# Optimization experiments

Hardware: AMD Instinct MI355X
Metric: run time of the kernel (lower is better)

Reference implementation:

```python
import math
import jax, jax.numpy as jnp
import numpy as np

H = 12
D = 64  # head dim

def _heads(x):
    # [b, n, h*d] -> [b, h, n, d]
    b, n, _ = x.shape
    return x.reshape(b, n, H, D).transpose(0, 2, 1, 3)

def setup_inputs() -> dict:
    key = jax.random.key(0)
    ks = jax.random.split(key, 9)
    hs = 768
    s = 1.0 / math.sqrt(hs)
    return {
        "query_states": jax.random.normal(ks[0], (8, 1024, hs), jnp.float32),
        "key_states": jax.random.normal(ks[1], (8, 1024, hs), jnp.float32),
        "Wd": jax.random.normal(ks[2], (hs, hs), jnp.float32) * s,
        "Wq": jax.random.normal(ks[3], (hs, hs), jnp.float32) * s,
        "bq": jax.random.normal(ks[4], (hs,), jnp.float32) * 0.01,
        "Wk": jax.random.normal(ks[5], (hs, hs), jnp.float32) * s,
        "bk": jax.random.normal(ks[6], (hs,), jnp.float32) * 0.01,
        "Wv": jax.random.normal(ks[7], (hs, hs), jnp.float32) * s,
        "bv": jax.random.normal(ks[8], (hs,), jnp.float32) * 0.01,
    }

def reference(query_states, key_states, Wd, Wq, bq, Wk, bk, Wv, bv):
    # projections (torch Linear: x @ W.T + b)
    qd = _heads(query_states @ Wd.T)          # [b,h,n,d]
    kd = _heads(key_states @ Wd.T)
    q = _heads(query_states @ Wq.T + bq)
    k = _heads(key_states @ Wk.T + bk)
    v = _heads(key_states @ Wv.T + bv)
    # -0.5 * cdist(qd, kd)^2 = -0.5*(|qd|^2 + |kd|^2) + qd@kd^T
    qd_sq = jnp.sum(qd * qd, axis=-1)          # [b,h,n]
    kd_sq = jnp.sum(kd * kd, axis=-1)          # [b,h,m]
    quad = (qd @ jnp.swapaxes(kd, -1, -2)
            - 0.5 * qd_sq[..., :, None]
            - 0.5 * kd_sq[..., None, :])       # [b,h,n,m]
    lin = q @ jnp.swapaxes(k, -1, -2)          # [b,h,n,m]
    scores = (quad + lin) / math.sqrt(D)
    probs = jax.nn.softmax(scores, axis=-1)
    ctx = probs @ v                            # [b,h,n,d]
    b, _, n, _ = ctx.shape
    return ctx.transpose(0, 2, 1, 3).reshape(b, n, H * D)
```

## Files before the change

### kernel.cpp

```cpp
#include <hip/hip_runtime.h>
#include <stdint.h>

typedef __attribute__((ext_vector_type(8))) short short8;
typedef __attribute__((ext_vector_type(4))) short short4v;
typedef __attribute__((ext_vector_type(4))) float f32x4;
typedef __attribute__((ext_vector_type(16))) float f32x16;
typedef __attribute__((ext_vector_type(4))) int int4v;

static __device__ __forceinline__ unsigned short f2b(float f) {
  unsigned int u = __builtin_bit_cast(unsigned int, f);
  u += 0x7fffu + ((u >> 16) & 1u);
  return (unsigned short)(u >> 16);
}
static __device__ __forceinline__ float b2f(unsigned short b) {
  unsigned int u = ((unsigned int)b) << 16;
  return __builtin_bit_cast(float, u);
}

#define GLD16(gp, lp)                                                          \
  __builtin_amdgcn_global_load_lds(                                            \
      (const __attribute__((address_space(1))) void*)(gp),                     \
      (__attribute__((address_space(3))) void*)(lp), 16, 0, 0)

#define MFMA16 __builtin_amdgcn_mfma_f32_16x16x32_bf16
#define MFMA32 __builtin_amdgcn_mfma_f32_32x32x16_bf16

#define CVTPK(dst, lo, hi)                                                     \
  asm("v_cvt_pk_bf16_f32 %0, %1, %2" : "=v"(dst) : "v"(lo), "v"(hi))
#define PLSWAP(x, y)                                                           \
  asm volatile("v_permlane32_swap_b32 %0, %1" : "+v"(x), "+v"(y))

#define QSC 0.18033688011112113f
#define C2 0.09016844005556057f

__global__ void cvtx_kernel(const float* __restrict__ q,
                            const float* __restrict__ k,
                            unsigned short* __restrict__ Xq,
                            unsigned short* __restrict__ Xk) {
  const int bx = blockIdx.x;
  const bool lo = bx < 6144;
  const float* src = lo ? q : k;
  unsigned short* dst = lo ? Xq : Xk;
  const int i = (lo ? bx : bx - 6144) * 256 + threadIdx.x;
  float4 v = reinterpret_cast<const float4*>(src)[i];
  short4v o;
  o.x = (short)f2b(v.x);
  o.y = (short)f2b(v.y);
  o.z = (short)f2b(v.z);
  o.w = (short)f2b(v.w);
  reinterpret_cast<short4v*>(dst)[i] = o;
}

__global__ void cvtw_kernel(const float* __restrict__ Wd,
                            const float* __restrict__ Wq,
                            const float* __restrict__ Wk,
                            const float* __restrict__ Wv,
                            unsigned short* __restrict__ Wcq,
                            unsigned short* __restrict__ Wck) {
  const int bx = blockIdx.x;
  const int seg = bx / 576;
  const int i = (bx - seg * 576) * 256 + threadIdx.x;
  const float* src;
  unsigned short* dst;
  switch (seg) {
    case 0: src = Wd; dst = Wcq; break;
    case 1: src = Wq; dst = Wcq + 589824; break;
    case 2: src = Wd; dst = Wck; break;
    case 3: src = Wk; dst = Wck + 589824; break;
    default: src = Wv; dst = Wck + 1179648; break;
  }
  float4 v = reinterpret_cast<const float4*>(src)[i];
  short4v o;
  o.x = (short)f2b(v.x);
  o.y = (short)f2b(v.y);
  o.z = (short)f2b(v.z);
  o.w = (short)f2b(v.w);
  reinterpret_cast<short4v*>(dst)[i] = o;
}

__global__ __launch_bounds__(512, 2) void proj_kernel(
    const unsigned short* __restrict__ Xq, const unsigned short* __restrict__ Xk,
    const unsigned short* __restrict__ Wcq, const unsigned short* __restrict__ Wck,
    const float* __restrict__ bq, const float* __restrict__ bk,
    const float* __restrict__ bv, unsigned short* __restrict__ Qc,
    unsigned short* __restrict__ Kc, unsigned short* __restrict__ Vt) {
  __shared__ __align__(16) short lds[3][2][256 * 32];
  const int by = blockIdx.y;
  const bool mode0 = (by < 6);
  const unsigned short* X = mode0 ? Xq : Xk;
  const unsigned short* W = mode0 ? Wcq : Wck;
  const int col0 = (mode0 ? by : by - 6) * 256;
  const int row0 = blockIdx.x * 256;
  const int tid = threadIdx.x;
  const int lane = tid & 63;
  const int wid = tid >> 6;
  const int wm = wid >> 2;
  const int wn = wid & 3;
  const int l15 = lane & 15, l4 = lane >> 4;
  const int RSWZ = (l4 ^ ((l15 >> 1) & 3)) << 4;

  f32x4 acc[8][4];
#pragma unroll
  for (int i = 0; i < 8; ++i)
#pragma unroll
    for (int j = 0; j < 4; ++j) acc[i][j] = (f32x4){0.f, 0.f, 0.f, 0.f};

  auto stage = [&](int bufi, int k0) {
#pragma unroll
    for (int iss = 0; iss < 2; ++iss) {
      const int c = iss * 512 + tid;
      const int r = c >> 2;
      const int sl = (c & 3) ^ ((c >> 3) & 3);
      const unsigned short* gp = X + (size_t)(row0 + r) * 768 + k0 + sl * 8;
      GLD16(gp, (char*)&lds[bufi][0][0] + (size_t)c * 16);
    }
#pragma unroll
    for (int iss = 0; iss < 2; ++iss) {
      const int c = iss * 512 + tid;
      const int r = c >> 2;
      const int sl = (c & 3) ^ ((c >> 3) & 3);
      const unsigned short* gp = W + (size_t)(col0 + r) * 768 + k0 + sl * 8;
      GLD16(gp, (char*)&lds[bufi][1][0] + (size_t)c * 16);
    }
  };

  stage(0, 0);
  stage(1, 32);

#pragma unroll 3
  for (int kt = 0; kt < 24; ++kt) {
    if (kt < 23) {
      asm volatile("s_waitcnt vmcnt(4) lgkmcnt(0)" ::: "memory");
    } else {
      asm volatile("s_waitcnt vmcnt(0) lgkmcnt(0)" ::: "memory");
    }
    __builtin_amdgcn_s_barrier();
    asm volatile("" ::: "memory");
    if (kt < 22) stage((kt + 2) % 3, (kt + 2) * 32);

    const char* Ab = (const char*)&lds[kt % 3][0][0];
    const char* Bb = (const char*)&lds[kt % 3][1][0];
    short8 a[8], b[4];
#pragma unroll
    for (int mt = 0; mt < 8; ++mt) {
      const int r = wm * 128 + mt * 16 + l15;
      a[mt] = *reinterpret_cast<const short8*>(Ab + r * 64 + RSWZ);
    }
#pragma unroll
    for (int nt = 0; nt < 4; ++nt) {
      const int r = wn * 64 + nt * 16 + l15;
      b[nt] = *reinterpret_cast<const short8*>(Bb + r * 64 + RSWZ);
    }
#pragma unroll
    for (int mt = 0; mt < 8; ++mt)
#pragma unroll
      for (int nt = 0; nt < 4; ++nt)
        acc[mt][nt] = MFMA16(a[mt], b[nt], acc[mt][nt], 0, 0, 0);
  }

  const int mat = mode0 ? (col0 >= 768 ? 1 : 0) : ((by - 6) / 3);
  const int cbase = col0 - mat * 768 + wn * 64;
  const float* barr = mode0 ? bq : (mat == 2 ? bv : bk);
  if (!mode0 && mat == 2) {
#pragma unroll
    for (int nt = 0; nt < 4; ++nt) {
      const int cc = cbase + nt * 16 + l15;
      const int hh = cc >> 6, dd = cc & 63;
      const float bias = barr[cc];
#pragma unroll
      for (int mt = 0; mt < 8; ++mt) {
        const int row = row0 + wm * 128 + mt * 16 + l4 * 4;
        const int bb = row >> 10, nn = row & 1023;
        short4v pv;
#pragma unroll
        for (int i = 0; i < 4; ++i)
          pv[i] = (short)f2b(acc[mt][nt][i] + bias);
        *reinterpret_cast<short4v*>(
            Vt + ((size_t)(bb * 12 + hh) * 64 + dd) * 1024 + nn) = pv;
      }
    }
  } else {
    const float scale = mode0 ? QSC : 1.0f;
    unsigned short* outC = mode0 ? Qc : Kc;
#pragma unroll
    for (int nt = 0; nt < 4; ++nt) {
      const int cc = cbase + nt * 16 + l15;
      const int hh = cc >> 6, dd = cc & 63;
      const float bias = (mat >= 1) ? barr[cc] : 0.f;
#pragma unroll
      for (int mt = 0; mt < 8; ++mt) {
#pragma unroll
        for (int i = 0; i < 4; ++i) {
          const int row = row0 + wm * 128 + mt * 16 + l4 * 4 + i;
          const int bb = row >> 10, nn = row & 1023;
          outC[((size_t)(bb * 12 + hh) * 1024 + nn) * 128 + mat * 64 + dd] =
              f2b((acc[mt][nt][i] + bias) * scale);
        }
      }
    }
  }
}

__global__ __launch_bounds__(256) void wv_kernel(
    const unsigned short* __restrict__ Kc, unsigned short* __restrict__ wq,
    const unsigned short* __restrict__ Vt, unsigned short* __restrict__ Vs) {
  __shared__ float wf[1024];
  const int bh = blockIdx.x;
  const int t = threadIdx.x;
  const int part = t & 3;
  const unsigned short* Kb = Kc + (size_t)bh * 1024 * 128;
#pragma unroll
  for (int it = 0; it < 16; ++it) {
    const int key = it * 64 + (t >> 2);
    const short8* p =
        reinterpret_cast<const short8*>(Kb + (size_t)key * 128 + part * 16);
    float s = 0.f;
    short8 x0 = p[0], x1 = p[1];
#pragma unroll
    for (int j = 0; j < 8; ++j) {
      const float f0 = b2f((unsigned short)x0[j]);
      const float f1 = b2f((unsigned short)x1[j]);
      s += f0 * f0 + f1 * f1;
    }
    s += __shfl_xor(s, 1);
    s += __shfl_xor(s, 2);
    if (part == 0) {
      const unsigned short wb = f2b(__builtin_amdgcn_exp2f(-s * C2));
      wf[key] = b2f(wb);
      wq[(size_t)bh * 1024 + key] = wb;
    }
  }
  __syncthreads();
  const unsigned short* Vb = Vt + (size_t)bh * 64 * 1024;
  unsigned short* Ob = Vs + (size_t)bh * 64 * 1024;
#pragma unroll
  for (int i = 0; i < 32; ++i) {
    const int e0 = (i * 256 + t) * 8;
    const int k0 = e0 & 1023;
    short8 v = *reinterpret_cast<const short8*>(Vb + e0);
#pragma unroll
    for (int j = 0; j < 8; ++j)
      v[j] = (short)f2b(b2f((unsigned short)v[j]) * wf[k0 + j]);
    *reinterpret_cast<short8*>(Ob + e0) = v;
  }
}

__global__ __launch_bounds__(256, 3) void attn_kernel(
    const unsigned short* __restrict__ Qc, const unsigned short* __restrict__ Kc,
    const unsigned short* __restrict__ Vs, const unsigned short* __restrict__ wq,
    float* __restrict__ out) {
  __shared__ __align__(16) short kbuf[2][64 * 128];
  __shared__ __align__(16) short vbuf[2][64 * 64];
  __shared__ __align__(16) short wbuf[1024];

  const int bh = blockIdx.x % 96;
  const int qb = blockIdx.x / 96;
  const int b = bh / 12, h = bh - b * 12;
  const int lane = threadIdx.x & 63;
  const int w = threadIdx.x >> 6;
  const int l31 = lane & 31, l5 = lane >> 5;

  const unsigned short* Kg = Kc + (size_t)bh * 1024 * 128;
  const unsigned short* Vg = Vs + (size_t)bh * 64 * 1024;

  auto stageK = [&](int bufi, int kb) {
#pragma unroll
    for (int i = 0; i < 4; ++i) {
      const int slot = i * 256 + threadIdx.x;
      const int row = slot >> 4;
      const int d0 = ((slot & 15) ^ (row & 15)) * 8;
      const unsigned short* gp = Kg + (size_t)(kb * 64 + row) * 128 + d0;
      GLD16(gp, (char*)(&kbuf[bufi][0]) + (i * 256 + w * 64) * 16);
    }
  };
  auto stageV = [&](int bufi, int kb) {
#pragma unroll
    for (int i = 0; i < 2; ++i) {
      const int slot = i * 256 + threadIdx.x;
      const int row = slot >> 3;
      const int k0 = ((slot & 7) ^ (row & 7)) * 8;
      const unsigned short* gp = Vg + (size_t)row * 1024 + kb * 64 + k0;
      GLD16(gp, (char*)(&vbuf[bufi][0]) + (i * 256 + w * 64) * 16);
    }
  };

  stageK(0, 0);
  stageV(0, 0);
  if (w < 2) {
    const unsigned short* gp = wq + (size_t)bh * 1024 + (w * 64 + lane) * 8;
    GLD16(gp, (char*)(&wbuf[0]) + w * 1024);
  }

  const unsigned short* Qb =
      Qc + ((size_t)bh * 1024 + qb * 128 + w * 32 + l31) * 128 + l5 * 8;
  short8 qf[8];
#pragma unroll
  for (int s = 0; s < 8; ++s)
    qf[s] = *reinterpret_cast<const short8*>(Qb + s * 16);

  f32x16 o0, o1, la;
#pragma unroll
  for (int r = 0; r < 16; ++r) {
    o0[r] = 0.f;
    o1[r] = 0.f;
    la[r] = 0.f;
  }
  float m = -1e30f;

  const int S4 = (lane & 15) << 4;
  const int S3 = (lane & 7) << 4;
  const int ko = l5 * 16;

  asm volatile("s_waitcnt vmcnt(0)" ::: "memory");
  __syncthreads();

  int buf = 0;
  for (int kb = 0; kb < 16; ++kb) {
    if (kb < 15) {
      stageK(buf ^ 1, kb + 1);
      stageV(buf ^ 1, kb + 1);
    }

    const char* kB = (const char*)(&kbuf[buf][0]) + l31 * 256;
    f32x16 s0, s1;
#pragma unroll
    for (int r = 0; r < 16; ++r) {
      s0[r] = 0.f;
      s1[r] = 0.f;
    }
#pragma unroll
    for (int s = 0; s < 8; ++s) {
      const int off = (s * 32 + ko) ^ S4;
      short8 a0 = *reinterpret_cast<const short8*>(kB + off);
      short8 a1 = *reinterpret_cast<const short8*>(kB + 8192 + off);
      s0 = MFMA32(a0, qf[s], s0, 0, 0, 0);
      s1 = MFMA32(a1, qf[s], s1, 0, 0, 0);
    }

    float mx = s0[0];
#pragma unroll
    for (int r = 1; r < 16; ++r) mx = fmaxf(mx, s0[r]);
#pragma unroll
    for (int r = 0; r < 16; ++r) mx = fmaxf(mx, s1[r]);
    mx = fmaxf(mx, __shfl_xor(mx, 32));

    if (!__all(mx <= m + 11.0f)) {
      const float mn = fmaxf(m, mx);
      const float c = __builtin_amdgcn_exp2f(m - mn);
      m = mn;
      float cr[16];
#pragma unroll
      for (int r = 0; r < 16; ++r)
        cr[r] = __shfl(c, (r & 3) + 8 * (r >> 2) + 4 * l5);
#pragma unroll
      for (int r = 0; r < 16; ++r) {
        la[r] *= cr[r];
        o0[r] *= cr[r];
        o1[r] *= cr[r];
      }
    }

#pragma unroll
    for (int r = 0; r < 16; ++r) {
      s0[r] = __builtin_amdgcn_exp2f(s0[r] - m);
      s1[r] = __builtin_amdgcn_exp2f(s1[r] - m);
    }
    unsigned int u[16];
#pragma unroll
    for (int j = 0; j < 8; ++j) {
      CVTPK(u[j], s0[2 * j], s0[2 * j + 1]);
      CVTPK(u[8 + j], s1[2 * j], s1[2 * j + 1]);
    }
    PLSWAP(u[0], u[2]);
    PLSWAP(u[1], u[3]);
    PLSWAP(u[4], u[6]);
    PLSWAP(u[5], u[7]);
    PLSWAP(u[8], u[10]);
    PLSWAP(u[9], u[11]);
    PLSWAP(u[12], u[14]);
    PLSWAP(u[13], u[15]);
    short8 pa[4];
    {
      int4v t0 = {(int)u[0], (int)u[1], (int)u[2], (int)u[3]};
      int4v t1 = {(int)u[4], (int)u[5], (int)u[6], (int)u[7]};
      int4v t2 = {(int)u[8], (int)u[9], (int)u[10], (int)u[11]};
      int4v t3 = {(int)u[12], (int)u[13], (int)u[14], (int)u[15]};
      pa[0] = __builtin_bit_cast(short8, t0);
      pa[1] = __builtin_bit_cast(short8, t1);
      pa[2] = __builtin_bit_cast(short8, t2);
      pa[3] = __builtin_bit_cast(short8, t3);
    }

    const char* vB = (const char*)(&vbuf[buf][0]) + l31 * 128;
    const char* wB = (const char*)(&wbuf[0]) + kb * 128 + ko;
#pragma unroll
    for (int kk = 0; kk < 4; ++kk) {
      const int off = (kk * 32 + ko) ^ S3;
      short8 v0 = *reinterpret_cast<const short8*>(vB + off);
      short8 v1 = *reinterpret_cast<const short8*>(vB + 4096 + off);
      short8 wf = *reinterpret_cast<const short8*>(wB + kk * 32);
      o0 = MFMA32(pa[kk], v0, o0, 0, 0, 0);
      o1 = MFMA32(pa[kk], v1, o1, 0, 0, 0);
      la = MFMA32(pa[kk], wf, la, 0, 0, 0);
    }

    asm volatile("s_waitcnt vmcnt(0)" ::: "memory");
    __syncthreads();
    buf ^= 1;
  }

  const int qbase = b * 1024 + qb * 128 + w * 32;
#pragma unroll
  for (int r = 0; r < 16; ++r) {
    const float iv = __builtin_amdgcn_rcpf(la[r]);
    const int q = qbase + (r & 3) + 8 * (r >> 2) + 4 * l5;
    float* op = out + (size_t)q * 768 + h * 64 + l31;
    op[0] = o0[r] * iv;
    op[32] = o1[r] * iv;
  }
}

extern "C" void kernel_launch(void* const* d_in, const int* in_sizes, int n_in,
                              void* d_out, int out_size, void* d_ws,
                              size_t ws_size, hipStream_t stream) {
  const float* query = (const float*)d_in[0];
  const float* key = (const float*)d_in[1];
  const float* Wd = (const float*)d_in[2];
  const float* Wq = (const float*)d_in[3];
  const float* bq = (const float*)d_in[4];
  const float* Wk = (const float*)d_in[5];
  const float* bk = (const float*)d_in[6];
  const float* Wv = (const float*)d_in[7];
  const float* bv = (const float*)d_in[8];
  float* out = (float*)d_out;

  char* p = (char*)d_ws;
  auto alloc = [&](size_t n) {
    char* r = p;
    p += (n + 255) & ~(size_t)255;
    return r;
  };
  unsigned short* Xq = (unsigned short*)alloc(8192ULL * 768 * 2);
  unsigned short* Xk = (unsigned short*)alloc(8192ULL * 768 * 2);
  unsigned short* Wcq = (unsigned short*)alloc(1536ULL * 768 * 2);
  unsigned short* Wck = (unsigned short*)alloc(2304ULL * 768 * 2);
  unsigned short* Qc = (unsigned short*)alloc(96ULL * 1024 * 128 * 2);
  unsigned short* Kc = (unsigned short*)alloc(96ULL * 1024 * 128 * 2);
  unsigned short* Vt = (unsigned short*)alloc(96ULL * 64 * 1024 * 2);
  unsigned short* wqv = (unsigned short*)alloc(96ULL * 1024 * 2);
  unsigned short* Vs = Xk;

  cvtx_kernel<<<12288, 256, 0, stream>>>(query, key, Xq, Xk);
  cvtw_kernel<<<2880, 256, 0, stream>>>(Wd, Wq, Wk, Wv, Wcq, Wck);

  proj_kernel<<<dim3(32, 15), 512, 0, stream>>>(Xq, Xk, Wcq, Wck, bq, bk, bv,
                                                Qc, Kc, Vt);

  wv_kernel<<<96, 256, 0, stream>>>(Kc, wqv, Vt, Vs);

  attn_kernel<<<768, 256, 0, stream>>>(Qc, Kc, Vs, wqv, out);
}
```

Before: 155.0 us.

## Split GEMM k-step into two phases with interleaved staging and MFMA priority

```diff
diff --git a/kernel.cpp b/kernel.cpp
--- a/kernel.cpp
+++ b/kernel.cpp
@@ -105,7 +105,7 @@
 #pragma unroll
     for (int j = 0; j < 4; ++j) acc[i][j] = (f32x4){0.f, 0.f, 0.f, 0.f};
 
-  auto stage = [&](int bufi, int k0) {
+  auto stageA = [&](int bufi, int k0) {
 #pragma unroll
     for (int iss = 0; iss < 2; ++iss) {
       const int c = iss * 512 + tid;
@@ -114,6 +114,8 @@
       const unsigned short* gp = X + (size_t)(row0 + r) * 768 + k0 + sl * 8;
       GLD16(gp, (char*)&lds[bufi][0][0] + (size_t)c * 16);
     }
+  };
+  auto stageB = [&](int bufi, int k0) {
 #pragma unroll
     for (int iss = 0; iss < 2; ++iss) {
       const int c = iss * 512 + tid;
@@ -124,8 +126,10 @@
     }
   };
 
-  stage(0, 0);
-  stage(1, 32);
+  stageA(0, 0);
+  stageB(0, 0);
+  stageA(1, 32);
+  stageB(1, 32);
 
 #pragma unroll 3
   for (int kt = 0; kt < 24; ++kt) {
@@ -136,13 +140,14 @@
     }
     __builtin_amdgcn_s_barrier();
     asm volatile("" ::: "memory");
-    if (kt < 22) stage((kt + 2) % 3, (kt + 2) * 32);
 
     const char* Ab = (const char*)&lds[kt % 3][0][0];
     const char* Bb = (const char*)&lds[kt % 3][1][0];
-    short8 a[8], b[4];
-#pragma unroll
-    for (int mt = 0; mt < 8; ++mt) {
+
+    if (kt < 22) stageA((kt + 2) % 3, (kt + 2) * 32);
+    short8 a[4], b[4];
+#pragma unroll
+    for (int mt = 0; mt < 4; ++mt) {
       const int r = wm * 128 + mt * 16 + l15;
       a[mt] = *reinterpret_cast<const short8*>(Ab + r * 64 + RSWZ);
     }
@@ -151,11 +156,32 @@
       const int r = wn * 64 + nt * 16 + l15;
       b[nt] = *reinterpret_cast<const short8*>(Bb + r * 64 + RSWZ);
     }
-#pragma unroll
-    for (int mt = 0; mt < 8; ++mt)
+    __builtin_amdgcn_s_barrier();
+    asm volatile("s_waitcnt lgkmcnt(0)" ::: "memory");
+    __builtin_amdgcn_s_setprio(1);
+#pragma unroll
+    for (int mt = 0; mt < 4; ++mt)
 #pragma unroll
       for (int nt = 0; nt < 4; ++nt)
         acc[mt][nt] = MFMA16(a[mt], b[nt], acc[mt][nt], 0, 0, 0);
+    __builtin_amdgcn_s_setprio(0);
+
+    short8 a2[4];
+#pragma unroll
+    for (int mt = 0; mt < 4; ++mt) {
+      const int r = wm * 128 + (mt + 4) * 16 + l15;
+      a2[mt] = *reinterpret_cast<const short8*>(Ab + r * 64 + RSWZ);
+    }
+    if (kt < 22) stageB((kt + 2) % 3, (kt + 2) * 32);
+    __builtin_amdgcn_s_barrier();
+    asm volatile("s_waitcnt lgkmcnt(0)" ::: "memory");
+    __builtin_amdgcn_s_setprio(1);
+#pragma unroll
+    for (int mt = 0; mt < 4; ++mt)
+#pragma unroll
+      for (int nt = 0; nt < 4; ++nt)
+        acc[mt + 4][nt] = MFMA16(a2[mt], b[nt], acc[mt + 4][nt], 0, 0, 0);
+    __builtin_amdgcn_s_setprio(0);
   }
 
   const int mat = mode0 ? (col0 >= 768 ? 1 : 0) : ((by - 6) / 3);
@@ -328,6 +354,7 @@
       s0[r] = 0.f;
       s1[r] = 0.f;
     }
+    __builtin_amdgcn_s_setprio(1);
 #pragma unroll
     for (int s = 0; s < 8; ++s) {
       const int off = (s * 32 + ko) ^ S4;
@@ -336,6 +363,7 @@
       s0 = MFMA32(a0, qf[s], s0, 0, 0, 0);
       s1 = MFMA32(a1, qf[s], s1, 0, 0, 0);
     }
+    __builtin_amdgcn_s_setprio(0);
 
     float mx = s0[0];
 #pragma unroll
@@ -393,6 +421,7 @@
 
     const char* vB = (const char*)(&vbuf[buf][0]) + l31 * 128;
     const char* wB = (const char*)(&wbuf[0]) + kb * 128 + ko;
+    __builtin_amdgcn_s_setprio(1);
 #pragma unroll
     for (int kk = 0; kk < 4; ++kk) {
       const int off = (kk * 32 + ko) ^ S3;
@@ -403,6 +432,7 @@
       o1 = MFMA32(pa[kk], v1, o1, 0, 0, 0);
       la = MFMA32(pa[kk], wf, la, 0, 0, 0);
     }
+    __builtin_amdgcn_s_setprio(0);
 
     asm volatile("s_waitcnt vmcnt(0)" ::: "memory");
     __syncthreads();
```

New measurement: 158.0 us. No clear change (+1.9%).
